# Optimization experiments

Measured on AMD Instinct MI355X. Metric: run time of the kernel, lower is better.

The kernel has to match this reference:

```python
import jax, jax.numpy as jnp
import numpy as np

NUM_GROUPS = 19  # cityscapes classes; groups in the grouped conv
GATES = 4
SLABS = 4  # hidden slabs per class


def setup_inputs() -> dict:
    key = jax.random.key(0)
    k1, k2, k3, k4, k5 = jax.random.split(key, 5)
    B, H, Wd = 4, 256, 512
    x = jax.random.normal(k1, (B, NUM_GROUPS, H, Wd), dtype=jnp.float32)
    h = jax.random.normal(k2, (B, NUM_GROUPS, SLABS, H, Wd), dtype=jnp.float32)
    c = jax.random.normal(k3, (B, NUM_GROUPS, SLABS, H, Wd), dtype=jnp.float32)
    # Conv2d(95 -> 304, k=3, groups=19): weight (304, 5, 3, 3), bias (304,)
    fan_in = 5 * 3 * 3
    bound = 1.0 / np.sqrt(fan_in)
    W = jax.random.uniform(k4, (4 * NUM_GROUPS * SLABS, 5, 3, 3), minval=-bound, maxval=bound, dtype=jnp.float32)
    b = jax.random.uniform(k5, (4 * NUM_GROUPS * SLABS,), minval=-bound, maxval=bound, dtype=jnp.float32)
    return {"x": x, "h": h, "c": c, "W": W, "b": b}


def reference(x, h, c, W, b):
    B, _, H, Wd = x.shape
    # Strided interleave: channel g*5+0 = x[:,g], g*5+1..4 = h[:,g,0..3]
    xh = jnp.concatenate([x[:, :, None], h], axis=2).reshape(B, NUM_GROUPS * 5, H, Wd)
    A = jax.lax.conv_general_dilated(
        xh, W, window_strides=(1, 1), padding=[(1, 1), (1, 1)],
        feature_group_count=NUM_GROUPS,
        dimension_numbers=("NCHW", "OIHW", "NCHW"))
    A = A + b[None, :, None, None]
    A = A.reshape(B, NUM_GROUPS, GATES, SLABS, H, Wd)
    i = jax.nn.sigmoid(A[:, :, 0])
    f = jax.nn.sigmoid(A[:, :, 1])
    o = jax.nn.sigmoid(A[:, :, 2])
    g = jnp.tanh(A[:, :, 3])
    new_c = f * c + i * g
    new_h = o * jnp.tanh(new_c)
    return (new_h, new_c)
```

## Files before the change

### kernel.cpp

```cpp
#include <hip/hip_runtime.h>
#include <hip/hip_bf16.h>

#define NG      19
#define HEIGHT  256
#define WIDTH   512
#define HW      (HEIGHT*WIDTH)
#define BATCH   4
#define TH      16
#define NT      4
#define HALO_R  18
#define HALO_CU 34
#define CH_U32  (HALO_R*HALO_CU)
#define LDS_U32 (5*CH_U32)
#define STAGE_TOT LDS_U32
#define STAGE_PER 12
#define WFRAG_SHORTS (NG*64*16)
#define BIAS_FLOATS (NG*16)

typedef __attribute__((ext_vector_type(8))) short short8;
typedef __attribute__((ext_vector_type(4))) float f32x4;
typedef __attribute__((ext_vector_type(2))) float f32x2;
typedef __attribute__((ext_vector_type(4))) unsigned int u32x4;

static __device__ __forceinline__ unsigned int bfbits(float f) {
    return (unsigned int)__builtin_bit_cast(unsigned short, __float2bfloat16(f));
}
static __device__ __forceinline__ unsigned int pack2(float lo, float hi) {
    return bfbits(lo) | (bfbits(hi) << 16);
}
static __device__ __forceinline__ unsigned int fsh16(unsigned int hi, unsigned int lo) {
    return (unsigned int)((((unsigned long long)hi << 32) | lo) >> 16);
}
static __device__ __forceinline__ float sig2(float a) {
    return __builtin_amdgcn_rcpf(1.0f + __builtin_amdgcn_exp2f(a));
}
static __device__ __forceinline__ float ftanh(float x) {
    return 2.0f * __builtin_amdgcn_rcpf(1.0f + __builtin_amdgcn_exp2f(-2.88539008f * x)) - 1.0f;
}

__global__ void wxform_kernel(const float* __restrict__ W,
                              const float* __restrict__ b,
                              short* __restrict__ wdst,
                              float* __restrict__ bdst) {
    int i = blockIdx.x * 256 + threadIdx.x;
    if (i < WFRAG_SHORTS) {
        int g   = i / 1024;
        int r   = i & 1023;
        int l   = r >> 4;
        int j   = r & 15;
        int q   = l >> 4;
        int row = l & 15;
        int s    = row >> 2;
        int gate = row & 3;
        int half = j >> 3;
        int jj   = j & 7;
        int m  = 8*half + 2*q + (jj >> 2);
        int kc = jj & 3;
        float wv = 0.0f;
        if (m <= 14 && kc < 3) {
            int ic = m / 3, kr = m % 3;
            int oc = g*16 + gate*4 + s;
            float scale = (gate == 3) ? -2.88539008f : -1.44269504f;
            wv = scale * W[((oc*5 + ic)*3 + kr)*3 + kc];
        }
        wdst[i] = (short)__builtin_bit_cast(unsigned short, __float2bfloat16(wv));
    } else if (i < WFRAG_SHORTS + BIAS_FLOATS) {
        int idx = i - WFRAG_SHORTS;
        int g = idx >> 4;
        int r = idx & 15;
        int s = r >> 2, gate = r & 3;
        float scale = (gate == 3) ? -2.88539008f : -1.44269504f;
        bdst[idx] = scale * b[g*16 + gate*4 + s];
    }
}

__launch_bounds__(256, 4)
__global__ void convlstm_mfma(const float* __restrict__ x,
                              const float* __restrict__ h,
                              const float* __restrict__ c,
                              const short* __restrict__ wfrag,
                              const float* __restrict__ biasp,
                              float* __restrict__ out) {
    __shared__ unsigned int lds[LDS_U32];

    const int t     = threadIdx.x;
    const int bid   = blockIdx.x;
    const int plane = bid >> 5;
    const int rem   = bid & 31;
    const int tr0   = (rem >> 1) * TH;
    const int tcb   = (rem & 1) * 256;
    const int g     = plane % NG;

    const int w  = t >> 6;
    const int l  = t & 63;
    const int q  = l >> 4;
    const int li = l & 15;

    const short8* ap = reinterpret_cast<const short8*>(wfrag + (g*64 + l)*16);
    const short8 a_lo = ap[0];
    const short8 a_hi = ap[1];
    f32x4 bias4;
    {
        float4 bv = *reinterpret_cast<const float4*>(biasp + g*16 + q*4);
        bias4[0] = bv.x; bias4[1] = bv.y; bias4[2] = bv.z; bias4[3] = bv.w;
    }

    const float* xb = x + plane * HW;
    const float* hb = h + (plane * 4) * HW;
    int soff[STAGE_PER];
    int meta[STAGE_PER];
    #pragma unroll
    for (int k = 0; k < STAGE_PER; ++k) {
        int p  = t + 256*k;
        int v  = (p < STAGE_TOT) ? 1 : 0;
        int pp = v ? p : 0;
        int ch = pp / CH_U32;
        int r2 = pp - ch*CH_U32;
        int r  = r2 / HALO_CU;
        int j2 = r2 - r*HALO_CU;
        int gr = tr0 + r - 1;
        int rok = ((unsigned)gr < HEIGHT) ? 1 : 0;
        int isx = (ch == 0) ? 1 : 0;
        soff[k] = (isx ? 0 : (ch-1)*HW) + gr*WIDTH + 2*j2 - 2;
        meta[k] = (ch*CH_U32 + r*HALO_CU + j2)
                | (v << 16) | (rok << 17)
                | ((j2 == 0) ? (1<<18) : 0) | ((j2 == 33) ? (1<<19) : 0)
                | (isx << 20);
    }

    int cbase[4];
    #pragma unroll
    for (int i = 0; i < 4; ++i) {
        int m = (i < 2) ? (2*q + i) : (8 + 2*q + (i - 2));
        if (m > 14) m = 14;
        cbase[i] = (m/3)*(CH_U32*4) + (m%3)*(HALO_CU*4) + 8*li;
    }
    const char* ldsb = reinterpret_cast<const char*>(lds);
    const int NC_OFF = BATCH * NG * 4 * HW;

    f32x2 pf[STAGE_PER];

    auto stage_issue = [&](int tc0) {
        const bool lt = (tc0 == 0), rt = (tc0 == 448);
        #pragma unroll
        for (int k = 0; k < STAGE_PER; ++k) {
            const int mk = meta[k];
            bool ok = (mk & (1<<16)) && (mk & (1<<17))
                   && !(lt && (mk & (1<<18))) && !(rt && (mk & (1<<19)));
            const float* bp = (mk & (1<<20)) ? xb : hb;
            f32x2 z; z[0] = 0.0f; z[1] = 0.0f;
            pf[k] = ok ? *reinterpret_cast<const f32x2*>(bp + soff[k] + tc0) : z;
        }
    };
    auto stage_write = [&]() {
        #pragma unroll
        for (int k = 0; k < STAGE_PER; ++k) {
            const int mk = meta[k];
            if (mk & (1<<16))
                lds[mk & 0xFFFF] = pack2(pf[k][0], pf[k][1]);
        }
    };

    stage_issue(tcb);
    stage_write();
    stage_issue(tcb + 64);
    asm volatile("s_waitcnt lgkmcnt(0)" ::: "memory");
    __builtin_amdgcn_s_barrier();
    asm volatile("" ::: "memory");

    #pragma unroll 1
    for (int tt = 0; tt < NT; ++tt) {
        const int tc0 = tcb + 64*tt;
        const int rowbase0 = (plane*4 + q)*HW + (tr0 + w*4)*WIDTH + tc0 + 4*li;

        f32x4 cp[4];
        #pragma unroll
        for (int tr4 = 0; tr4 < 4; ++tr4)
            cp[tr4] = __builtin_nontemporal_load(
                reinterpret_cast<const f32x4*>(c + rowbase0 + tr4*WIDTH));

        #pragma unroll
        for (int tr4 = 0; tr4 < 4; ++tr4) {
            const int tr = w*4 + tr4;
            uint2 dv[4][2];
            #pragma unroll
            for (int i = 0; i < 4; ++i) {
                const uint2* pp2 = reinterpret_cast<const uint2*>(
                    ldsb + cbase[i] + tr*(HALO_CU*4));
                dv[i][0] = pp2[0];
                dv[i][1] = pp2[1];
            }
            float nh4[4], nc4[4];
            #pragma unroll
            for (int n = 0; n < 4; ++n) {
                u32x4 blo_u, bhi_u;
                #pragma unroll
                for (int i = 0; i < 4; ++i) {
                    const unsigned d0 = dv[i][0].x, d1 = dv[i][0].y;
                    const unsigned d2 = dv[i][1].x, d3 = dv[i][1].y;
                    unsigned w0, w1;
                    if (n == 0)      { w0 = fsh16(d1,d0); w1 = fsh16(d2,d1); }
                    else if (n == 1) { w0 = d1;           w1 = d2;           }
                    else if (n == 2) { w0 = fsh16(d2,d1); w1 = fsh16(d3,d2); }
                    else             { w0 = d2;           w1 = d3;           }
                    if (i < 2) { blo_u[2*i]     = w0; blo_u[2*i+1]     = w1; }
                    else       { bhi_u[2*(i-2)] = w0; bhi_u[2*(i-2)+1] = w1; }
                }
                const short8 blo = __builtin_bit_cast(short8, blo_u);
                const short8 bhi = __builtin_bit_cast(short8, bhi_u);

                f32x4 acc = bias4;
                acc = __builtin_amdgcn_mfma_f32_16x16x32_bf16(a_lo, blo, acc, 0, 0, 0);
                acc = __builtin_amdgcn_mfma_f32_16x16x32_bf16(a_hi, bhi, acc, 0, 0, 0);

                const float cv = cp[tr4][n];
                const float iv = sig2(acc[0]);
                const float fv = sig2(acc[1]);
                const float ov = sig2(acc[2]);
                const float gv = 2.0f * sig2(acc[3]) - 1.0f;
                const float nc = fv * cv + iv * gv;
                nc4[n] = nc;
                nh4[n] = ov * ftanh(nc);
            }
            const int rowchan = rowbase0 + tr4*WIDTH;
            f32x4 nhv; nhv[0]=nh4[0]; nhv[1]=nh4[1]; nhv[2]=nh4[2]; nhv[3]=nh4[3];
            f32x4 ncv; ncv[0]=nc4[0]; ncv[1]=nc4[1]; ncv[2]=nc4[2]; ncv[3]=nc4[3];
            __builtin_nontemporal_store(nhv, reinterpret_cast<f32x4*>(out + rowchan));
            __builtin_nontemporal_store(ncv, reinterpret_cast<f32x4*>(out + NC_OFF + rowchan));
        }

        if (tt + 1 < NT) {
            asm volatile("" ::: "memory");
            __builtin_amdgcn_s_barrier();
            asm volatile("" ::: "memory");
            stage_write();
            if (tt + 2 < NT) stage_issue(tcb + 64*(tt + 2));
            asm volatile("s_waitcnt lgkmcnt(0)" ::: "memory");
            __builtin_amdgcn_s_barrier();
            asm volatile("" ::: "memory");
        }
    }
}

extern "C" void kernel_launch(void* const* d_in, const int* in_sizes, int n_in,
                              void* d_out, int out_size, void* d_ws, size_t ws_size,
                              hipStream_t stream) {
    (void)in_sizes; (void)n_in; (void)out_size; (void)ws_size;
    const float* x = (const float*)d_in[0];
    const float* h = (const float*)d_in[1];
    const float* c = (const float*)d_in[2];
    const float* W = (const float*)d_in[3];
    const float* b = (const float*)d_in[4];
    float* out = (float*)d_out;

    short* wdst = (short*)d_ws;
    float* bdst = (float*)((char*)d_ws + WFRAG_SHORTS * sizeof(short));

    hipLaunchKernelGGL(wxform_kernel,
                       dim3((WFRAG_SHORTS + BIAS_FLOATS + 255) / 256), dim3(256),
                       0, stream, W, b, wdst, bdst);
    hipLaunchKernelGGL(convlstm_mfma, dim3(BATCH * NG * 32), dim3(256),
                       0, stream, x, h, c, (const short*)wdst, bdst, out);
}
```

Measured before the change: 144.0 us.

## Double-buffer LDS tiles, prefetch c one tile ahead, and merge gate reciprocals

Splits LDS into two staging buffers and fully unrolls the four column tiles, so each iteration needs one barrier instead of two. The c values for the next tile are also prefetched while the current tile computes. The LSTM gate math is rewritten algebraically so the sigmoid and tanh reciprocals are combined into two rcp calls per pixel instead of six. The cost is double the LDS, more registers, and occupancy lowered to 3 blocks per CU via launch bounds.

```diff
diff --git a/kernel.cpp b/kernel.cpp
--- a/kernel.cpp
+++ b/kernel.cpp
@@ -30,12 +30,6 @@
 }
 static __device__ __forceinline__ unsigned int fsh16(unsigned int hi, unsigned int lo) {
     return (unsigned int)((((unsigned long long)hi << 32) | lo) >> 16);
-}
-static __device__ __forceinline__ float sig2(float a) {
-    return __builtin_amdgcn_rcpf(1.0f + __builtin_amdgcn_exp2f(a));
-}
-static __device__ __forceinline__ float ftanh(float x) {
-    return 2.0f * __builtin_amdgcn_rcpf(1.0f + __builtin_amdgcn_exp2f(-2.88539008f * x)) - 1.0f;
 }
 
 __global__ void wxform_kernel(const float* __restrict__ W,
@@ -74,14 +68,14 @@
     }
 }
 
-__launch_bounds__(256, 4)
+__launch_bounds__(256, 3)
 __global__ void convlstm_mfma(const float* __restrict__ x,
                               const float* __restrict__ h,
                               const float* __restrict__ c,
                               const short* __restrict__ wfrag,
                               const float* __restrict__ biasp,
                               float* __restrict__ out) {
-    __shared__ unsigned int lds[LDS_U32];
+    __shared__ unsigned int lds[2][LDS_U32];
 
     const int t     = threadIdx.x;
     const int bid   = blockIdx.x;
@@ -135,7 +129,6 @@
         if (m > 14) m = 14;
         cbase[i] = (m/3)*(CH_U32*4) + (m%3)*(HALO_CU*4) + 8*li;
     }
-    const char* ldsb = reinterpret_cast<const char*>(lds);
     const int NC_OFF = BATCH * NG * 4 * HW;
 
     f32x2 pf[STAGE_PER];
@@ -152,33 +145,25 @@
             pf[k] = ok ? *reinterpret_cast<const f32x2*>(bp + soff[k] + tc0) : z;
         }
     };
-    auto stage_write = [&]() {
+    auto stage_write = [&](unsigned int* buf) {
         #pragma unroll
         for (int k = 0; k < STAGE_PER; ++k) {
             const int mk = meta[k];
             if (mk & (1<<16))
-                lds[mk & 0xFFFF] = pack2(pf[k][0], pf[k][1]);
-        }
-    };
-
-    stage_issue(tcb);
-    stage_write();
-    stage_issue(tcb + 64);
-    asm volatile("s_waitcnt lgkmcnt(0)" ::: "memory");
-    __builtin_amdgcn_s_barrier();
-    asm volatile("" ::: "memory");
-
-    #pragma unroll 1
-    for (int tt = 0; tt < NT; ++tt) {
-        const int tc0 = tcb + 64*tt;
+                buf[mk & 0xFFFF] = pack2(pf[k][0], pf[k][1]);
+        }
+    };
+    auto cload = [&](int tc0, f32x4 (&cp)[4]) {
         const int rowbase0 = (plane*4 + q)*HW + (tr0 + w*4)*WIDTH + tc0 + 4*li;
-
-        f32x4 cp[4];
         #pragma unroll
         for (int tr4 = 0; tr4 < 4; ++tr4)
             cp[tr4] = __builtin_nontemporal_load(
                 reinterpret_cast<const f32x4*>(c + rowbase0 + tr4*WIDTH));
-
+    };
+
+    auto do_tile = [&](int tc0, const unsigned int* buf, const f32x4 (&cp)[4]) {
+        const char* ldsb = reinterpret_cast<const char*>(buf);
+        const int rowbase0 = (plane*4 + q)*HW + (tr0 + w*4)*WIDTH + tc0 + 4*li;
         #pragma unroll
         for (int tr4 = 0; tr4 < 4; ++tr4) {
             const int tr = w*4 + tr4;
@@ -214,13 +199,19 @@
                 acc = __builtin_amdgcn_mfma_f32_16x16x32_bf16(a_hi, bhi, acc, 0, 0, 0);
 
                 const float cv = cp[tr4][n];
-                const float iv = sig2(acc[0]);
-                const float fv = sig2(acc[1]);
-                const float ov = sig2(acc[2]);
-                const float gv = 2.0f * sig2(acc[3]) - 1.0f;
-                const float nc = fv * cv + iv * gv;
+                const float u  = __builtin_amdgcn_exp2f(acc[0]);
+                const float v  = __builtin_amdgcn_exp2f(acc[1]);
+                const float wo = __builtin_amdgcn_exp2f(acc[2]);
+                const float z  = __builtin_amdgcn_exp2f(acc[3]);
+                const float pu = 1.0f + u, pv = 1.0f + v;
+                const float pw = 1.0f + wo, pz = 1.0f + z;
+                const float puz = pu * pz;
+                const float r1  = __builtin_amdgcn_rcpf(pv * puz);
+                const float nc  = fmaf(cv, puz, (1.0f - z) * pv) * r1;
+                const float tt2 = __builtin_amdgcn_exp2f(-2.88539008f * nc);
+                const float r2  = __builtin_amdgcn_rcpf(pw * (1.0f + tt2));
                 nc4[n] = nc;
-                nh4[n] = ov * ftanh(nc);
+                nh4[n] = (1.0f - tt2) * r2;
             }
             const int rowchan = rowbase0 + tr4*WIDTH;
             f32x4 nhv; nhv[0]=nh4[0]; nhv[1]=nh4[1]; nhv[2]=nh4[2]; nhv[3]=nh4[3];
@@ -228,18 +219,42 @@
             __builtin_nontemporal_store(nhv, reinterpret_cast<f32x4*>(out + rowchan));
             __builtin_nontemporal_store(ncv, reinterpret_cast<f32x4*>(out + NC_OFF + rowchan));
         }
-
-        if (tt + 1 < NT) {
-            asm volatile("" ::: "memory");
-            __builtin_amdgcn_s_barrier();
-            asm volatile("" ::: "memory");
-            stage_write();
-            if (tt + 2 < NT) stage_issue(tcb + 64*(tt + 2));
-            asm volatile("s_waitcnt lgkmcnt(0)" ::: "memory");
-            __builtin_amdgcn_s_barrier();
-            asm volatile("" ::: "memory");
-        }
-    }
+    };
+
+    f32x4 cpA[4], cpB[4];
+
+    stage_issue(tcb);
+    stage_write(lds[0]);
+    stage_issue(tcb + 64);
+    cload(tcb,      cpA);
+    cload(tcb + 64, cpB);
+    asm volatile("s_waitcnt lgkmcnt(0)" ::: "memory");
+    __builtin_amdgcn_s_barrier();
+    asm volatile("" ::: "memory");
+
+    do_tile(tcb, lds[0], cpA);
+    stage_write(lds[1]);
+    stage_issue(tcb + 128);
+    cload(tcb + 128, cpA);
+    asm volatile("s_waitcnt lgkmcnt(0)" ::: "memory");
+    __builtin_amdgcn_s_barrier();
+    asm volatile("" ::: "memory");
+
+    do_tile(tcb + 64, lds[1], cpB);
+    stage_write(lds[0]);
+    stage_issue(tcb + 192);
+    cload(tcb + 192, cpB);
+    asm volatile("s_waitcnt lgkmcnt(0)" ::: "memory");
+    __builtin_amdgcn_s_barrier();
+    asm volatile("" ::: "memory");
+
+    do_tile(tcb + 128, lds[0], cpA);
+    stage_write(lds[1]);
+    asm volatile("s_waitcnt lgkmcnt(0)" ::: "memory");
+    __builtin_amdgcn_s_barrier();
+    asm volatile("" ::: "memory");
+
+    do_tile(tcb + 192, lds[1], cpB);
 }
 
 extern "C" void kernel_launch(void* const* d_in, const int* in_sizes, int n_in,
```

New measurement: 143.4 us. About the same (-0.4%).
